# Kernel tuning notes

Hardware: AMD Instinct MI355X
Metric: run time of the kernel (lower is better)

The kernel has to match this reference:

```python
import jax, jax.numpy as jnp
import numpy as np

HEADS = 8

def setup_inputs() -> dict:
    key = jax.random.key(0)
    ks = jax.random.split(key, 6)
    N, C, L = 8, 512, 2048
    s = 0.02
    return {
        'x':  jax.random.normal(ks[0], (N, C, L), dtype=jnp.float32),
        'Wq': jax.random.normal(ks[1], (C, C), dtype=jnp.float32) * s,
        'Wk': jax.random.normal(ks[2], (C, C), dtype=jnp.float32) * s,
        'Wv': jax.random.normal(ks[3], (C, C), dtype=jnp.float32) * s,
        'Wo': jax.random.normal(ks[4], (C, C), dtype=jnp.float32) * s,
        'bo': jnp.zeros((C,), dtype=jnp.float32),
    }

def reference(x, Wq, Wk, Wv, Wo, bo):
    N, C, L = x.shape
    h = HEADS
    d = C // h
    scale = C ** (-0.5)  # note: scales by full channels, as in the original

    def proj(W):
        # Conv1d(k=1, bias=False) == per-position linear: [N,C,L] -> [N,L,h,d]
        y = jnp.einsum('oc,ncl->nlo', W, x)
        return y.reshape(N, L, h, d)

    q, k, v = proj(Wq), proj(Wk), proj(Wv)

    qk = jnp.einsum('nqhd,nkhd->nhqk', q, k)  # [N,h,L,L]
    causal_mask = jnp.tril(jnp.ones((L, L), dtype=bool))
    qk = jnp.where(causal_mask, qk, -jnp.inf)
    attn = jax.nn.softmax(qk * scale, axis=-1)

    out = jnp.einsum('nhqk,nkhd->nqhd', attn, v)  # [N,L,h,d]
    out = out.reshape(N, L, C).transpose(0, 2, 1)  # n (h d) l
    return jnp.einsum('oc,ncl->nol', Wo, out) + bo[None, :, None]
```

## Files before the change

kernel.cpp:

```cpp
#include <hip/hip_runtime.h>
#include <math.h>

typedef __bf16 bf16;
typedef __attribute__((ext_vector_type(8))) __bf16 bf16x8;
typedef __attribute__((ext_vector_type(4))) float f32x4;
typedef unsigned short u16;
typedef unsigned int u32;

constexpr int Nn = 8, Cc = 512, Ll = 2048, Hh = 8, Dd = 64;
constexpr float kScale = 0.044194173824159216f;
constexpr float kQexp2 = kScale * 1.44269504088896341f;
constexpr size_t NCL = (size_t)Nn * Cc * Ll;
constexpr size_t WSZ = (size_t)Cc * Cc;

static __device__ __forceinline__ u16 bfbits(bf16 v) {
    union { bf16 b; u16 u; } x; x.b = v; return x.u;
}
static __device__ __forceinline__ u32 fbits(float f) {
    union { float f; u32 u; } x; x.f = f; return x.u;
}
static __device__ __forceinline__ float fexp2(float x) {
#if __has_builtin(__builtin_amdgcn_exp2f)
    return __builtin_amdgcn_exp2f(x);
#else
    return exp2f(x);
#endif
}

#define MFMA(a, b, c) __builtin_amdgcn_mfma_f32_16x16x32_bf16((a), (b), (c), 0, 0, 0)

static __device__ __forceinline__ void async16(const bf16* g, bf16* l) {
    __builtin_amdgcn_global_load_lds(
        (const __attribute__((address_space(1))) void*)g,
        (__attribute__((address_space(3))) void*)l, 16, 0, 0);
}

__global__ __launch_bounds__(256) void prep_kernel(
    const float* __restrict__ x,
    const float* __restrict__ Wq, const float* __restrict__ Wk,
    const float* __restrict__ Wv, const float* __restrict__ Wo,
    bf16* __restrict__ xT, bf16* __restrict__ Wb)
{
    const int tid = threadIdx.x;
    if (blockIdx.z == Nn) {
        int gid = (blockIdx.y * 32 + blockIdx.x) * 256 + tid;
        int w = gid >> 14;
        int o = (gid & 16383) * 4;
        const float* src = (w == 0) ? Wq : (w == 1) ? Wk : (w == 2) ? Wv : Wo;
        bf16* dst = Wb + (size_t)w * WSZ;
#pragma unroll
        for (int j = 0; j < 4; j++) {
            float4 v = ((const float4*)src)[o + j];
            ushort4 u;
            u.x = bfbits((bf16)v.x); u.y = bfbits((bf16)v.y);
            u.z = bfbits((bf16)v.z); u.w = bfbits((bf16)v.w);
            *(ushort4*)(dst + (size_t)(o + j) * 4) = u;
        }
        return;
    }

    __shared__ bf16 Ts[64][72];
    const int lt = blockIdx.x, ct = blockIdx.y, n = blockIdx.z;

    const int cr = tid >> 2, l0 = (tid & 3) * 16;
    const float* src = x + ((size_t)(n * Cc + ct * 64 + cr)) * Ll + lt * 64 + l0;
#pragma unroll
    for (int i = 0; i < 4; i++) {
        float4 v = *(const float4*)(src + i * 4);
        Ts[l0 + i * 4 + 0][cr] = (bf16)v.x;
        Ts[l0 + i * 4 + 1][cr] = (bf16)v.y;
        Ts[l0 + i * 4 + 2][cr] = (bf16)v.z;
        Ts[l0 + i * 4 + 3][cr] = (bf16)v.w;
    }
    __syncthreads();

    const int lr = tid >> 2, c0 = (tid & 3) * 16;
    bf16* dst = xT + ((size_t)(n * Ll + lt * 64 + lr)) * Cc + ct * 64 + c0;
    *(bf16x8*)(dst)     = *(const bf16x8*)&Ts[lr][c0];
    *(bf16x8*)(dst + 8) = *(const bf16x8*)&Ts[lr][c0 + 8];
}

__global__ __launch_bounds__(256) void qkv_gemm(
    const bf16* __restrict__ xT, const bf16* __restrict__ Wb,
    bf16* __restrict__ Qt, bf16* __restrict__ Kt, bf16* __restrict__ Vb)
{
    const int lt = blockIdx.x, ow = blockIdx.y, n = blockIdx.z;
    const int widx = ow >> 2, otile = ow & 3;

    __shared__ bf16 Xs[128 * 64];
    __shared__ bf16 Ws[128 * 64];

    const int tid = threadIdx.x;
    const int lane = tid & 63, wv = tid >> 6;
    const int m = lane & 15, quad = lane >> 4;
    const int rh = wv & 1, ch = wv >> 1;

    const bf16* __restrict__ W = Wb + (size_t)widx * WSZ + (size_t)otile * 128 * Cc;
    const bf16* __restrict__ X = xT + (size_t)(n * Ll + lt * 128) * Cc;

    int srow[4], scol[4];
#pragma unroll
    for (int i = 0; i < 4; i++) {
        int q = i * 256 + tid;
        srow[i] = q >> 3;
        scol[i] = ((q ^ (q >> 3)) & 7) * 8;
    }

    f32x4 acc[4][4] = {};

    for (int c0 = 0; c0 < Cc; c0 += 64) {
#pragma unroll
        for (int i = 0; i < 4; i++)
            async16(&X[(size_t)srow[i] * Cc + c0 + scol[i]], &Xs[(i * 256 + tid) * 8]);
#pragma unroll
        for (int i = 0; i < 4; i++)
            async16(&W[(size_t)srow[i] * Cc + c0 + scol[i]], &Ws[(i * 256 + tid) * 8]);
        __syncthreads();

        const bf16* TA = (widx < 2) ? Xs : Ws;
        const bf16* TB = (widx < 2) ? Ws : Xs;
#pragma unroll
        for (int kk = 0; kk < 2; kk++) {
            const int sw = (((kk * 4 + quad) ^ (m & 7)) * 8);
            bf16x8 af[4], bfr[4];
#pragma unroll
            for (int t = 0; t < 4; t++)
                af[t] = *(const bf16x8*)&TA[(rh * 64 + t * 16 + m) * 64 + sw];
#pragma unroll
            for (int u = 0; u < 4; u++)
                bfr[u] = *(const bf16x8*)&TB[(ch * 64 + u * 16 + m) * 64 + sw];
#pragma unroll
            for (int t = 0; t < 4; t++)
#pragma unroll
                for (int u = 0; u < 4; u++)
                    acc[t][u] = MFMA(af[t], bfr[u], acc[t][u]);
        }
        __syncthreads();
    }

    if (widx < 2) {
        const float fq = (widx == 0) ? kQexp2 : 1.0f;
        bf16* __restrict__ OUT = (widx == 0) ? Qt : Kt;
#pragma unroll
        for (int u = 0; u < 4; u++) {
            const int o = otile * 128 + ch * 64 + u * 16 + m;
            const int h = o >> 6, d = o & 63;
            bf16* base = OUT + (size_t)(n * Hh + h) * Ll * Dd + d;
#pragma unroll
            for (int t = 0; t < 4; t++) {
                const int l0 = lt * 128 + rh * 64 + t * 16 + quad * 4;
#pragma unroll
                for (int r = 0; r < 4; r++)
                    base[(size_t)(l0 + r) * Dd] = (bf16)(acc[t][u][r] * fq);
            }
        }
    } else {
#pragma unroll
        for (int t = 0; t < 4; t++) {
            const int ob = otile * 128 + rh * 64 + t * 16 + quad * 4;
#pragma unroll
            for (int r = 0; r < 4; r++) {
                const int oo = ob + r, h = oo >> 6, d = oo & 63;
                bf16* base = Vb + ((size_t)(n * Hh + h) * Dd + d) * Ll;
#pragma unroll
                for (int u = 0; u < 4; u++)
                    base[lt * 128 + ch * 64 + u * 16 + m] = (bf16)acc[t][u][r];
            }
        }
    }
}

__global__ __launch_bounds__(256, 4) void attn_mfma(
    const bf16* __restrict__ Qt, const bf16* __restrict__ Kt,
    const bf16* __restrict__ Vb, bf16* __restrict__ AO)
{
    const int h  = blockIdx.x;
    const int jp = blockIdx.y;
    const int n  = blockIdx.z;

    __shared__ bf16 KV[2][2][64 * 64];
    __shared__ bf16 Pbuf[4][16 * 64];

    const int tid = threadIdx.x;
    const int lane = tid & 63, wv = tid >> 6;
    const int m = lane & 15, quad = lane >> 4;

    const size_t bnh = (size_t)(n * Hh + h) * Ll * Dd;
    const bf16* __restrict__ Qh = Qt + bnh;
    const bf16* __restrict__ Kh = Kt + bnh;
    const bf16* __restrict__ Vh = Vb + bnh;

    const int srow = tid >> 3;
    const int scs  = (((tid & 7) ^ (srow & 7)) * 8);
    const int swz  = (m & 7);

    bf16* const Pw = &Pbuf[wv][0];

    bf16x8 ones;
#pragma unroll
    for (int j = 0; j < 8; j++) ones[j] = (bf16)1.0f;

    const int thr = 16 * wv;
    int koff[4];
#pragma unroll
    for (int r = 0; r < 4; r++) koff[r] = quad * 4 + r - m;

#pragma unroll 1
    for (int ph = 0; ph < 2; ph++) {
        const int st = ph ? (31 - jp) : jp;
        const int nk = st + 1;
        const int qrow0 = st * 64 + wv * 16;

        bf16x8 qf0 = *(const bf16x8*)&Qh[(size_t)(qrow0 + m) * Dd + quad * 8];
        bf16x8 qf1 = *(const bf16x8*)&Qh[(size_t)(qrow0 + m) * Dd + 32 + quad * 8];

        f32x4 O[4] = {};
        f32x4 Ls = {};

        async16(&Kh[(size_t)(srow) * Dd + scs],      &KV[0][0][(size_t)tid * 8]);
        async16(&Kh[(size_t)(srow + 32) * Dd + scs], &KV[0][0][(size_t)tid * 8 + 2048]);
        async16(&Vh[(size_t)srow * Ll + scs],        &KV[0][1][(size_t)tid * 8]);
        async16(&Vh[(size_t)(srow + 32) * Ll + scs], &KV[0][1][(size_t)tid * 8 + 2048]);
        __syncthreads();

        for (int kt = 0; kt < nk; kt++) {
            const int cur = kt & 1;

            if (kt + 1 < nk) {
                const int kn = (kt + 1) * 64;
                async16(&Kh[(size_t)(kn + srow) * Dd + scs],      &KV[cur ^ 1][0][(size_t)tid * 8]);
                async16(&Kh[(size_t)(kn + srow + 32) * Dd + scs], &KV[cur ^ 1][0][(size_t)tid * 8 + 2048]);
                async16(&Vh[(size_t)srow * Ll + kn + scs],        &KV[cur ^ 1][1][(size_t)tid * 8]);
                async16(&Vh[(size_t)(srow + 32) * Ll + kn + scs], &KV[cur ^ 1][1][(size_t)tid * 8 + 2048]);
            }

            const bf16* Ks = &KV[cur][0][0];
            const bf16* Vs = &KV[cur][1][0];

            f32x4 St[4] = {};
#pragma unroll
            for (int t = 0; t < 4; t++) {
                bf16x8 kf0 = *(const bf16x8*)&Ks[(t * 16 + m) * 64 + ((quad ^ swz) * 8)];
                bf16x8 kf1 = *(const bf16x8*)&Ks[(t * 16 + m) * 64 + (((4 + quad) ^ swz) * 8)];
                St[t] = MFMA(kf0, qf0, St[t]);
                St[t] = MFMA(kf1, qf1, St[t]);
            }

            const bool dg = (kt == st);
#pragma unroll
            for (int t = 0; t < 4; t++) {
                float p0 = fexp2(St[t][0]);
                float p1 = fexp2(St[t][1]);
                float p2 = fexp2(St[t][2]);
                float p3 = fexp2(St[t][3]);
                if (dg) {
                    if (t * 16 + koff[0] > thr) p0 = 0.f;
                    if (t * 16 + koff[1] > thr) p1 = 0.f;
                    if (t * 16 + koff[2] > thr) p2 = 0.f;
                    if (t * 16 + koff[3] > thr) p3 = 0.f;
                }
                u32 pk0 = (fbits(p0) >> 16) | (fbits(p1) & 0xFFFF0000u);
                u32 pk1 = (fbits(p2) >> 16) | (fbits(p3) & 0xFFFF0000u);
                const int pidx = m * 64 + (((2 * t + (quad >> 1)) ^ swz) * 8) + (quad & 1) * 4;
                *(uint2*)&Pw[pidx] = make_uint2(pk0, pk1);
            }
            asm volatile("s_waitcnt lgkmcnt(0)" ::: "memory");

            bf16x8 pf0 = *(const bf16x8*)&Pw[m * 64 + ((quad ^ swz) * 8)];
            bf16x8 pf1 = *(const bf16x8*)&Pw[m * 64 + (((4 + quad) ^ swz) * 8)];

            Ls = MFMA(pf0, ones, Ls);
            Ls = MFMA(pf1, ones, Ls);
#pragma unroll
            for (int t = 0; t < 4; t++) {
                bf16x8 vf0 = *(const bf16x8*)&Vs[(t * 16 + m) * 64 + ((quad ^ swz) * 8)];
                bf16x8 vf1 = *(const bf16x8*)&Vs[(t * 16 + m) * 64 + (((4 + quad) ^ swz) * 8)];
                O[t] = MFMA(pf0, vf0, O[t]);
                O[t] = MFMA(pf1, vf1, O[t]);
            }

            __syncthreads();
        }

        f32x4 inv;
#pragma unroll
        for (int r = 0; r < 4; r++) inv[r] = 1.0f / Ls[r];

        const size_t aobase = (size_t)n * Ll * Cc + (size_t)h * 64;
#pragma unroll
        for (int t = 0; t < 4; t++)
#pragma unroll
            for (int r = 0; r < 4; r++) {
                const int q = qrow0 + quad * 4 + r;
                AO[aobase + (size_t)q * Cc + t * 16 + m] = (bf16)(O[t][r] * inv[r]);
            }
    }
}

__global__ __launch_bounds__(256) void out_gemm(
    const bf16* __restrict__ AO, const bf16* __restrict__ Wb,
    const float* __restrict__ bo, float* __restrict__ out)
{
    const int lt = blockIdx.x, ot = blockIdx.y, n = blockIdx.z;

    __shared__ bf16 Ws[128 * 64];
    __shared__ bf16 Bs[128 * 64];

    const int tid = threadIdx.x;
    const int lane = tid & 63, wv = tid >> 6;
    const int m = lane & 15, quad = lane >> 4;
    const int rh = wv & 1, ch = wv >> 1;

    const bf16* __restrict__ W = Wb + 3 * WSZ + (size_t)ot * 128 * Cc;
    const bf16* __restrict__ B = AO + (size_t)(n * Ll + lt * 128) * Cc;

    int srow[4], scol[4];
#pragma unroll
    for (int i = 0; i < 4; i++) {
        int q = i * 256 + tid;
        srow[i] = q >> 3;
        scol[i] = ((q ^ (q >> 3)) & 7) * 8;
    }

    f32x4 acc[4][4] = {};

    for (int c0 = 0; c0 < Cc; c0 += 64) {
#pragma unroll
        for (int i = 0; i < 4; i++)
            async16(&W[(size_t)srow[i] * Cc + c0 + scol[i]], &Ws[(i * 256 + tid) * 8]);
#pragma unroll
        for (int i = 0; i < 4; i++)
            async16(&B[(size_t)srow[i] * Cc + c0 + scol[i]], &Bs[(i * 256 + tid) * 8]);
        __syncthreads();

#pragma unroll
        for (int kk = 0; kk < 2; kk++) {
            const int sw = (((kk * 4 + quad) ^ (m & 7)) * 8);
            bf16x8 af[4], bfr[4];
#pragma unroll
            for (int t = 0; t < 4; t++)
                af[t] = *(const bf16x8*)&Ws[(rh * 64 + t * 16 + m) * 64 + sw];
#pragma unroll
            for (int u = 0; u < 4; u++)
                bfr[u] = *(const bf16x8*)&Bs[(ch * 64 + u * 16 + m) * 64 + sw];
#pragma unroll
            for (int t = 0; t < 4; t++)
#pragma unroll
                for (int u = 0; u < 4; u++)
                    acc[t][u] = MFMA(af[t], bfr[u], acc[t][u]);
        }
        __syncthreads();
    }

#pragma unroll
    for (int t = 0; t < 4; t++) {
        const int ob = ot * 128 + rh * 64 + t * 16 + quad * 4;
#pragma unroll
        for (int r = 0; r < 4; r++) {
            const int o = ob + r;
            const float b = bo[o];
            float* base = out + ((size_t)n * Cc + o) * Ll + lt * 128 + ch * 64;
#pragma unroll
            for (int u = 0; u < 4; u++)
                base[u * 16 + m] = acc[t][u][r] + b;
        }
    }
}

extern "C" void kernel_launch(void* const* d_in, const int* in_sizes, int n_in,
                              void* d_out, int out_size, void* d_ws, size_t ws_size,
                              hipStream_t stream)
{
    const float* x  = (const float*)d_in[0];
    const float* Wq = (const float*)d_in[1];
    const float* Wk = (const float*)d_in[2];
    const float* Wv = (const float*)d_in[3];
    const float* Wo = (const float*)d_in[4];
    const float* bo = (const float*)d_in[5];
    float* out = (float*)d_out;

    bf16* ws = (bf16*)d_ws;
    bf16* xT = ws;
    bf16* Wb = xT + NCL;
    bf16* Qt = Wb + 4 * WSZ;
    bf16* Kt = Qt + NCL;
    bf16* Vb = Kt + NCL;
    bf16* AO = Vb + NCL;

    prep_kernel<<<dim3(32, 8, Nn + 1), 256, 0, stream>>>(x, Wq, Wk, Wv, Wo, xT, Wb);
    qkv_gemm<<<dim3(16, 12, Nn), 256, 0, stream>>>(xT, Wb, Qt, Kt, Vb);
    attn_mfma<<<dim3(Hh, 16, Nn), 256, 0, stream>>>(Qt, Kt, Vb, AO);
    out_gemm<<<dim3(16, 4, Nn), 256, 0, stream>>>(AO, Wb, bo, out);
}
```

Baseline: 195.0 us.

## Enlarge attention query tile to 128 rows with two 16-row groups per wave

Each attention block now handles 128 query rows instead of 64, with each wave owning 32 rows split into two 16-row groups that share every K and V fragment loaded from LDS. The grid halves along the query dimension, and each wave skips key tiles beyond its own diagonal. The intent is to reuse each staged K/V tile across twice as many queries, halving global and LDS traffic per query. In exchange it uses more registers and LDS, lowers the occupancy hint to 2, launches fewer blocks, and lets waves go idle on diagonal tiles they skip.

```diff
diff --git a/kernel.cpp b/kernel.cpp
--- a/kernel.cpp
+++ b/kernel.cpp
@@ -170,7 +170,7 @@
     }
 }
 
-__global__ __launch_bounds__(256, 4) void attn_mfma(
+__global__ __launch_bounds__(256, 2) void attn_mfma(
     const bf16* __restrict__ Qt, const bf16* __restrict__ Kt,
     const bf16* __restrict__ Vb, bf16* __restrict__ AO)
 {
@@ -179,7 +179,7 @@
     const int n  = blockIdx.z;
 
     __shared__ bf16 KV[2][2][64 * 64];
-    __shared__ bf16 Pbuf[4][16 * 64];
+    __shared__ bf16 Pbuf[4][32 * 64];
 
     const int tid = threadIdx.x;
     const int lane = tid & 63, wv = tid >> 6;
@@ -200,22 +200,28 @@
 #pragma unroll
     for (int j = 0; j < 8; j++) ones[j] = (bf16)1.0f;
 
-    const int thr = 16 * wv;
+    const int thr0 = (wv & 1) * 32;
+    const int doff = wv >> 1;
     int koff[4];
 #pragma unroll
     for (int r = 0; r < 4; r++) koff[r] = quad * 4 + r - m;
 
 #pragma unroll 1
     for (int ph = 0; ph < 2; ph++) {
-        const int st = ph ? (31 - jp) : jp;
-        const int nk = st + 1;
-        const int qrow0 = st * 64 + wv * 16;
-
-        bf16x8 qf0 = *(const bf16x8*)&Qh[(size_t)(qrow0 + m) * Dd + quad * 8];
-        bf16x8 qf1 = *(const bf16x8*)&Qh[(size_t)(qrow0 + m) * Dd + 32 + quad * 8];
-
-        f32x4 O[4] = {};
-        f32x4 Ls = {};
+        const int st = ph ? (15 - jp) : jp;
+        const int nk = 2 * st + 2;
+        const int dtile = 2 * st + doff;
+        const int qrow0 = st * 128 + wv * 32;
+
+        bf16x8 qf[2][2];
+#pragma unroll
+        for (int g = 0; g < 2; g++) {
+            qf[g][0] = *(const bf16x8*)&Qh[(size_t)(qrow0 + g * 16 + m) * Dd + quad * 8];
+            qf[g][1] = *(const bf16x8*)&Qh[(size_t)(qrow0 + g * 16 + m) * Dd + 32 + quad * 8];
+        }
+
+        f32x4 O[4][2] = {};
+        f32x4 Ls[2] = {};
 
         async16(&Kh[(size_t)(srow) * Dd + scs],      &KV[0][0][(size_t)tid * 8]);
         async16(&Kh[(size_t)(srow + 32) * Dd + scs], &KV[0][0][(size_t)tid * 8 + 2048]);
@@ -234,66 +240,84 @@
                 async16(&Vh[(size_t)(srow + 32) * Ll + kn + scs], &KV[cur ^ 1][1][(size_t)tid * 8 + 2048]);
             }
 
-            const bf16* Ks = &KV[cur][0][0];
-            const bf16* Vs = &KV[cur][1][0];
-
-            f32x4 St[4] = {};
-#pragma unroll
-            for (int t = 0; t < 4; t++) {
-                bf16x8 kf0 = *(const bf16x8*)&Ks[(t * 16 + m) * 64 + ((quad ^ swz) * 8)];
-                bf16x8 kf1 = *(const bf16x8*)&Ks[(t * 16 + m) * 64 + (((4 + quad) ^ swz) * 8)];
-                St[t] = MFMA(kf0, qf0, St[t]);
-                St[t] = MFMA(kf1, qf1, St[t]);
+            if (kt <= dtile) {
+                const bf16* Ks = &KV[cur][0][0];
+                const bf16* Vs = &KV[cur][1][0];
+
+                f32x4 St[4][2] = {};
+#pragma unroll
+                for (int t = 0; t < 4; t++) {
+                    bf16x8 kf0 = *(const bf16x8*)&Ks[(t * 16 + m) * 64 + ((quad ^ swz) * 8)];
+                    bf16x8 kf1 = *(const bf16x8*)&Ks[(t * 16 + m) * 64 + (((4 + quad) ^ swz) * 8)];
+#pragma unroll
+                    for (int g = 0; g < 2; g++) {
+                        St[t][g] = MFMA(kf0, qf[g][0], St[t][g]);
+                        St[t][g] = MFMA(kf1, qf[g][1], St[t][g]);
+                    }
+                }
+
+                const bool dg = (kt == dtile);
+#pragma unroll
+                for (int g = 0; g < 2; g++) {
+                    const int thr = thr0 + g * 16;
+#pragma unroll
+                    for (int t = 0; t < 4; t++) {
+                        float p0 = fexp2(St[t][g][0]);
+                        float p1 = fexp2(St[t][g][1]);
+                        float p2 = fexp2(St[t][g][2]);
+                        float p3 = fexp2(St[t][g][3]);
+                        if (dg) {
+                            if (t * 16 + koff[0] > thr) p0 = 0.f;
+                            if (t * 16 + koff[1] > thr) p1 = 0.f;
+                            if (t * 16 + koff[2] > thr) p2 = 0.f;
+                            if (t * 16 + koff[3] > thr) p3 = 0.f;
+                        }
+                        u32 pk0 = (fbits(p0) >> 16) | (fbits(p1) & 0xFFFF0000u);
+                        u32 pk1 = (fbits(p2) >> 16) | (fbits(p3) & 0xFFFF0000u);
+                        const int pidx = (g * 16 + m) * 64 +
+                                         (((2 * t + (quad >> 1)) ^ swz) * 8) + (quad & 1) * 4;
+                        *(uint2*)&Pw[pidx] = make_uint2(pk0, pk1);
+                    }
+                }
+                asm volatile("s_waitcnt lgkmcnt(0)" ::: "memory");
+
+                bf16x8 pf[2][2];
+#pragma unroll
+                for (int g = 0; g < 2; g++) {
+                    pf[g][0] = *(const bf16x8*)&Pw[(g * 16 + m) * 64 + ((quad ^ swz) * 8)];
+                    pf[g][1] = *(const bf16x8*)&Pw[(g * 16 + m) * 64 + (((4 + quad) ^ swz) * 8)];
+                    Ls[g] = MFMA(pf[g][0], ones, Ls[g]);
+                    Ls[g] = MFMA(pf[g][1], ones, Ls[g]);
+                }
+#pragma unroll
+                for (int t = 0; t < 4; t++) {
+                    bf16x8 vf0 = *(const bf16x8*)&Vs[(t * 16 + m) * 64 + ((quad ^ swz) * 8)];
+                    bf16x8 vf1 = *(const bf16x8*)&Vs[(t * 16 + m) * 64 + (((4 + quad) ^ swz) * 8)];
+#pragma unroll
+                    for (int g = 0; g < 2; g++) {
+                        O[t][g] = MFMA(pf[g][0], vf0, O[t][g]);
+                        O[t][g] = MFMA(pf[g][1], vf1, O[t][g]);
+                    }
+                }
             }
 
-            const bool dg = (kt == st);
-#pragma unroll
-            for (int t = 0; t < 4; t++) {
-                float p0 = fexp2(St[t][0]);
-                float p1 = fexp2(St[t][1]);
-                float p2 = fexp2(St[t][2]);
-                float p3 = fexp2(St[t][3]);
-                if (dg) {
-                    if (t * 16 + koff[0] > thr) p0 = 0.f;
-                    if (t * 16 + koff[1] > thr) p1 = 0.f;
-                    if (t * 16 + koff[2] > thr) p2 = 0.f;
-                    if (t * 16 + koff[3] > thr) p3 = 0.f;
+            __syncthreads();
+        }
+
+        const size_t aobase = (size_t)n * Ll * Cc + (size_t)h * 64;
+#pragma unroll
+        for (int g = 0; g < 2; g++) {
+            f32x4 inv;
+#pragma unroll
+            for (int r = 0; r < 4; r++) inv[r] = 1.0f / Ls[g][r];
+#pragma unroll
+            for (int t = 0; t < 4; t++)
+#pragma unroll
+                for (int r = 0; r < 4; r++) {
+                    const int q = qrow0 + g * 16 + quad * 4 + r;
+                    AO[aobase + (size_t)q * Cc + t * 16 + m] = (bf16)(O[t][g][r] * inv[r]);
                 }
-                u32 pk0 = (fbits(p0) >> 16) | (fbits(p1) & 0xFFFF0000u);
-                u32 pk1 = (fbits(p2) >> 16) | (fbits(p3) & 0xFFFF0000u);
-                const int pidx = m * 64 + (((2 * t + (quad >> 1)) ^ swz) * 8) + (quad & 1) * 4;
-                *(uint2*)&Pw[pidx] = make_uint2(pk0, pk1);
-            }
-            asm volatile("s_waitcnt lgkmcnt(0)" ::: "memory");
-
-            bf16x8 pf0 = *(const bf16x8*)&Pw[m * 64 + ((quad ^ swz) * 8)];
-            bf16x8 pf1 = *(const bf16x8*)&Pw[m * 64 + (((4 + quad) ^ swz) * 8)];
-
-            Ls = MFMA(pf0, ones, Ls);
-            Ls = MFMA(pf1, ones, Ls);
-#pragma unroll
-            for (int t = 0; t < 4; t++) {
-                bf16x8 vf0 = *(const bf16x8*)&Vs[(t * 16 + m) * 64 + ((quad ^ swz) * 8)];
-                bf16x8 vf1 = *(const bf16x8*)&Vs[(t * 16 + m) * 64 + (((4 + quad) ^ swz) * 8)];
-                O[t] = MFMA(pf0, vf0, O[t]);
-                O[t] = MFMA(pf1, vf1, O[t]);
-            }
-
-            __syncthreads();
-        }
-
-        f32x4 inv;
-#pragma unroll
-        for (int r = 0; r < 4; r++) inv[r] = 1.0f / Ls[r];
-
-        const size_t aobase = (size_t)n * Ll * Cc + (size_t)h * 64;
-#pragma unroll
-        for (int t = 0; t < 4; t++)
-#pragma unroll
-            for (int r = 0; r < 4; r++) {
-                const int q = qrow0 + quad * 4 + r;
-                AO[aobase + (size_t)q * Cc + t * 16 + m] = (bf16)(O[t][r] * inv[r]);
-            }
+        }
     }
 }
 
@@ -389,6 +413,6 @@
 
     prep_kernel<<<dim3(32, 8, Nn + 1), 256, 0, stream>>>(x, Wq, Wk, Wv, Wo, xT, Wb);
     qkv_gemm<<<dim3(16, 12, Nn), 256, 0, stream>>>(xT, Wb, Qt, Kt, Vb);
-    attn_mfma<<<dim3(Hh, 16, Nn), 256, 0, stream>>>(Qt, Kt, Vb, AO);
+    attn_mfma<<<dim3(Hh, 8, Nn), 256, 0, stream>>>(Qt, Kt, Vb, AO);
     out_gemm<<<dim3(16, 4, Nn), 256, 0, stream>>>(AO, Wb, bo, out);
 }
```

New measurement: 195.2 us. Within noise of the previous version (+0.1%).

## Use 32x32 MFMA attention with register-resident P and 128-row query tiles

Applied to the files above, without the earlier changes.

Rewrites the attention kernel to use 32x32x16 bf16 MFMA. The softmax probabilities stay in registers: they are packed with v_cvt_pk_bf16_f32 and rearranged with v_permlane32_swap, replacing the LDS round trip through a P buffer. Each block now handles a 128-row query tile in one pass, where before it handled two 64-row tiles paired for load balance. The row sums are accumulated with scalar adds rather than an MFMA against a ones vector. This removes LDS traffic and extra MFMAs per key tile, but per-block work is now uneven; blocks are ordered heaviest-first to offset that.

```diff
diff --git a/kernel.cpp b/kernel.cpp
--- a/kernel.cpp
+++ b/kernel.cpp
@@ -4,6 +4,7 @@
 typedef __bf16 bf16;
 typedef __attribute__((ext_vector_type(8))) __bf16 bf16x8;
 typedef __attribute__((ext_vector_type(4))) float f32x4;
+typedef __attribute__((ext_vector_type(16))) float f32x16;
 typedef unsigned short u16;
 typedef unsigned int u32;
 
@@ -15,9 +16,6 @@
 
 static __device__ __forceinline__ u16 bfbits(bf16 v) {
     union { bf16 b; u16 u; } x; x.b = v; return x.u;
-}
-static __device__ __forceinline__ u32 fbits(float f) {
-    union { float f; u32 u; } x; x.f = f; return x.u;
 }
 static __device__ __forceinline__ float fexp2(float x) {
 #if __has_builtin(__builtin_amdgcn_exp2f)
@@ -28,11 +26,21 @@
 }
 
 #define MFMA(a, b, c) __builtin_amdgcn_mfma_f32_16x16x32_bf16((a), (b), (c), 0, 0, 0)
+#define MFMA32(a, b, c) __builtin_amdgcn_mfma_f32_32x32x16_bf16((a), (b), (c), 0, 0, 0)
 
 static __device__ __forceinline__ void async16(const bf16* g, bf16* l) {
     __builtin_amdgcn_global_load_lds(
         (const __attribute__((address_space(1))) void*)g,
         (__attribute__((address_space(3))) void*)l, 16, 0, 0);
+}
+
+static __device__ __forceinline__ u32 cvtpk(float lo, float hi) {
+    u32 d;
+    asm("v_cvt_pk_bf16_f32 %0, %1, %2" : "=v"(d) : "v"(lo), "v"(hi));
+    return d;
+}
+static __device__ __forceinline__ void swap32(u32& d, u32& s) {
+    asm volatile("v_permlane32_swap_b32 %0, %1" : "+v"(d), "+v"(s));
 }
 
 __global__ __launch_bounds__(256) void prep_kernel(
@@ -175,15 +183,16 @@
     const bf16* __restrict__ Vb, bf16* __restrict__ AO)
 {
     const int h  = blockIdx.x;
-    const int jp = blockIdx.y;
+    const int st = 15 - (int)blockIdx.y;
     const int n  = blockIdx.z;
 
     __shared__ bf16 KV[2][2][64 * 64];
-    __shared__ bf16 Pbuf[4][16 * 64];
+    __shared__ float Lsc[4][32];
 
     const int tid = threadIdx.x;
     const int lane = tid & 63, wv = tid >> 6;
-    const int m = lane & 15, quad = lane >> 4;
+    const int l31 = lane & 31, hb = lane >> 5;
+    const int sw7 = l31 & 7;
 
     const size_t bnh = (size_t)(n * Hh + h) * Ll * Dd;
     const bf16* __restrict__ Qh = Qt + bnh;
@@ -192,108 +201,116 @@
 
     const int srow = tid >> 3;
     const int scs  = (((tid & 7) ^ (srow & 7)) * 8);
-    const int swz  = (m & 7);
-
-    bf16* const Pw = &Pbuf[wv][0];
-
-    bf16x8 ones;
-#pragma unroll
-    for (int j = 0; j < 8; j++) ones[j] = (bf16)1.0f;
-
-    const int thr = 16 * wv;
-    int koff[4];
-#pragma unroll
-    for (int r = 0; r < 4; r++) koff[r] = quad * 4 + r - m;
-
-#pragma unroll 1
-    for (int ph = 0; ph < 2; ph++) {
-        const int st = ph ? (31 - jp) : jp;
-        const int nk = st + 1;
-        const int qrow0 = st * 64 + wv * 16;
-
-        bf16x8 qf0 = *(const bf16x8*)&Qh[(size_t)(qrow0 + m) * Dd + quad * 8];
-        bf16x8 qf1 = *(const bf16x8*)&Qh[(size_t)(qrow0 + m) * Dd + 32 + quad * 8];
-
-        f32x4 O[4] = {};
-        f32x4 Ls = {};
-
-        async16(&Kh[(size_t)(srow) * Dd + scs],      &KV[0][0][(size_t)tid * 8]);
-        async16(&Kh[(size_t)(srow + 32) * Dd + scs], &KV[0][0][(size_t)tid * 8 + 2048]);
-        async16(&Vh[(size_t)srow * Ll + scs],        &KV[0][1][(size_t)tid * 8]);
-        async16(&Vh[(size_t)(srow + 32) * Ll + scs], &KV[0][1][(size_t)tid * 8 + 2048]);
-        __syncthreads();
-
-        for (int kt = 0; kt < nk; kt++) {
-            const int cur = kt & 1;
-
-            if (kt + 1 < nk) {
-                const int kn = (kt + 1) * 64;
-                async16(&Kh[(size_t)(kn + srow) * Dd + scs],      &KV[cur ^ 1][0][(size_t)tid * 8]);
-                async16(&Kh[(size_t)(kn + srow + 32) * Dd + scs], &KV[cur ^ 1][0][(size_t)tid * 8 + 2048]);
-                async16(&Vh[(size_t)srow * Ll + kn + scs],        &KV[cur ^ 1][1][(size_t)tid * 8]);
-                async16(&Vh[(size_t)(srow + 32) * Ll + kn + scs], &KV[cur ^ 1][1][(size_t)tid * 8 + 2048]);
-            }
-
+
+    const int nk    = 2 * st + 2;
+    const int dtile = 2 * st + (wv >> 1);
+    const int mhalf = wv & 1;
+    const int qrow0 = st * 128 + wv * 32;
+
+    bf16x8 qf[4];
+#pragma unroll
+    for (int s = 0; s < 4; s++)
+        qf[s] = *(const bf16x8*)&Qh[(size_t)(qrow0 + l31) * Dd + s * 16 + hb * 8];
+
+    f32x16 O0 = {}, O1 = {};
+    float Lacc = 0.f;
+
+    async16(&Kh[(size_t)srow * Dd + scs],        &KV[0][0][(size_t)tid * 8]);
+    async16(&Kh[(size_t)(srow + 32) * Dd + scs], &KV[0][0][(size_t)tid * 8 + 2048]);
+    async16(&Vh[(size_t)srow * Ll + scs],        &KV[0][1][(size_t)tid * 8]);
+    async16(&Vh[(size_t)(srow + 32) * Ll + scs], &KV[0][1][(size_t)tid * 8 + 2048]);
+    __syncthreads();
+
+    for (int kt = 0; kt < nk; kt++) {
+        const int cur = kt & 1;
+
+        if (kt + 1 < nk) {
+            const int kn = (kt + 1) * 64;
+            async16(&Kh[(size_t)(kn + srow) * Dd + scs],      &KV[cur ^ 1][0][(size_t)tid * 8]);
+            async16(&Kh[(size_t)(kn + srow + 32) * Dd + scs], &KV[cur ^ 1][0][(size_t)tid * 8 + 2048]);
+            async16(&Vh[(size_t)srow * Ll + kn + scs],        &KV[cur ^ 1][1][(size_t)tid * 8]);
+            async16(&Vh[(size_t)(srow + 32) * Ll + kn + scs], &KV[cur ^ 1][1][(size_t)tid * 8 + 2048]);
+        }
+
+        if (kt <= dtile) {
             const bf16* Ks = &KV[cur][0][0];
             const bf16* Vs = &KV[cur][1][0];
-
-            f32x4 St[4] = {};
-#pragma unroll
-            for (int t = 0; t < 4; t++) {
-                bf16x8 kf0 = *(const bf16x8*)&Ks[(t * 16 + m) * 64 + ((quad ^ swz) * 8)];
-                bf16x8 kf1 = *(const bf16x8*)&Ks[(t * 16 + m) * 64 + (((4 + quad) ^ swz) * 8)];
-                St[t] = MFMA(kf0, qf0, St[t]);
-                St[t] = MFMA(kf1, qf1, St[t]);
+            const bool dg = (kt == dtile);
+
+#pragma unroll
+            for (int i = 0; i < 2; i++) {
+                if (i == 1 && dg && mhalf == 0) continue;
+
+                f32x16 St = {};
+#pragma unroll
+                for (int s = 0; s < 4; s++) {
+                    bf16x8 kfs = *(const bf16x8*)
+                        &Ks[(32 * i + l31) * 64 + (((2 * s + hb) ^ sw7) * 8)];
+                    St = MFMA32(kfs, qf[s], St);
+                }
+
+                const bool msk = dg && (i == mhalf);
+
+#pragma unroll
+                for (int s = 0; s < 2; s++) {
+                    const int c0 = 4 * i + 2 * s + hb;
+                    bf16x8 v0 = *(const bf16x8*)&Vs[l31 * 64 + ((c0 ^ sw7) * 8)];
+                    bf16x8 v1 = *(const bf16x8*)&Vs[(32 + l31) * 64 + ((c0 ^ sw7) * 8)];
+
+                    float p[8];
+#pragma unroll
+                    for (int j = 0; j < 8; j++) {
+                        const int r = s * 8 + j;
+                        float pv = fexp2(St[r]);
+                        if (msk) {
+                            const int kc = (r & 3) + 8 * (r >> 2) + 4 * hb;
+                            if (kc > l31) pv = 0.f;
+                        }
+                        p[j] = pv;
+                    }
+                    Lacc += ((p[0] + p[1]) + (p[2] + p[3]))
+                          + ((p[4] + p[5]) + (p[6] + p[7]));
+
+                    u32 A = cvtpk(p[0], p[1]);
+                    u32 B = cvtpk(p[2], p[3]);
+                    u32 C = cvtpk(p[4], p[5]);
+                    u32 D = cvtpk(p[6], p[7]);
+                    swap32(A, C);
+                    swap32(B, D);
+                    union { u32 w[4]; bf16x8 v; } pu;
+                    pu.w[0] = A; pu.w[1] = B; pu.w[2] = C; pu.w[3] = D;
+
+                    O0 = MFMA32(pu.v, v0, O0);
+                    O1 = MFMA32(pu.v, v1, O1);
+                }
             }
-
-            const bool dg = (kt == st);
-#pragma unroll
-            for (int t = 0; t < 4; t++) {
-                float p0 = fexp2(St[t][0]);
-                float p1 = fexp2(St[t][1]);
-                float p2 = fexp2(St[t][2]);
-                float p3 = fexp2(St[t][3]);
-                if (dg) {
-                    if (t * 16 + koff[0] > thr) p0 = 0.f;
-                    if (t * 16 + koff[1] > thr) p1 = 0.f;
-                    if (t * 16 + koff[2] > thr) p2 = 0.f;
-                    if (t * 16 + koff[3] > thr) p3 = 0.f;
-                }
-                u32 pk0 = (fbits(p0) >> 16) | (fbits(p1) & 0xFFFF0000u);
-                u32 pk1 = (fbits(p2) >> 16) | (fbits(p3) & 0xFFFF0000u);
-                const int pidx = m * 64 + (((2 * t + (quad >> 1)) ^ swz) * 8) + (quad & 1) * 4;
-                *(uint2*)&Pw[pidx] = make_uint2(pk0, pk1);
-            }
-            asm volatile("s_waitcnt lgkmcnt(0)" ::: "memory");
-
-            bf16x8 pf0 = *(const bf16x8*)&Pw[m * 64 + ((quad ^ swz) * 8)];
-            bf16x8 pf1 = *(const bf16x8*)&Pw[m * 64 + (((4 + quad) ^ swz) * 8)];
-
-            Ls = MFMA(pf0, ones, Ls);
-            Ls = MFMA(pf1, ones, Ls);
-#pragma unroll
-            for (int t = 0; t < 4; t++) {
-                bf16x8 vf0 = *(const bf16x8*)&Vs[(t * 16 + m) * 64 + ((quad ^ swz) * 8)];
-                bf16x8 vf1 = *(const bf16x8*)&Vs[(t * 16 + m) * 64 + (((4 + quad) ^ swz) * 8)];
-                O[t] = MFMA(pf0, vf0, O[t]);
-                O[t] = MFMA(pf1, vf1, O[t]);
-            }
-
-            __syncthreads();
-        }
-
-        f32x4 inv;
-#pragma unroll
-        for (int r = 0; r < 4; r++) inv[r] = 1.0f / Ls[r];
+        }
+
+        __syncthreads();
+    }
+
+    {
+        float u = Lacc, w = Lacc;
+        {
+            u32 uu, ww;
+            __builtin_memcpy(&uu, &u, 4);
+            __builtin_memcpy(&ww, &w, 4);
+            swap32(uu, ww);
+            __builtin_memcpy(&u, &uu, 4);
+            __builtin_memcpy(&w, &ww, 4);
+        }
+        const float Ltot = u + w;
+        Lsc[wv][l31] = Ltot;
 
         const size_t aobase = (size_t)n * Ll * Cc + (size_t)h * 64;
 #pragma unroll
-        for (int t = 0; t < 4; t++)
-#pragma unroll
-            for (int r = 0; r < 4; r++) {
-                const int q = qrow0 + quad * 4 + r;
-                AO[aobase + (size_t)q * Cc + t * 16 + m] = (bf16)(O[t][r] * inv[r]);
-            }
+        for (int r = 0; r < 16; r++) {
+            const int qr = (r & 3) + 8 * (r >> 2) + 4 * hb;
+            const float inv = 1.0f / Lsc[wv][qr];
+            const size_t row = aobase + (size_t)(qrow0 + qr) * Cc;
+            AO[row + l31]      = (bf16)(O0[r] * inv);
+            AO[row + 32 + l31] = (bf16)(O1[r] * inv);
+        }
     }
 }
 
```

Result: slower. 209.2 us (+7.3%).
